# Optimization experiments

Measured on AMD Instinct MI355X. Metric: run time of the kernel, lower is better.

## Reference

```python
import jax, jax.numpy as jnp
import numpy as np

B, S, D_IN = 4, 2048, 2048
H, HD, G = 16, 128, 4
D_OUT = H * HD  # 2048
EPS = 1e-6
NEG_INF = -1e9


def zc_rmsnorm(x, scale):
    # zero-centered RMSNorm, computed in fp32
    xf = x.astype(jnp.float32)
    rms = jax.lax.rsqrt(jnp.mean(xf * xf, axis=-1, keepdims=True) + EPS)
    return (xf * rms * (1.0 + scale)).astype(x.dtype)


def rope(x, cos, sin):
    # x: (b, h, s, d); cos/sin: (s, d) -> broadcast over (b, h)
    d = x.shape[-1]
    x1, x2 = x[..., : d // 2], x[..., d // 2 :]
    rotated = jnp.concatenate([-x2, x1], axis=-1)
    return x * cos[None, None] + rotated * sin[None, None]


def setup_inputs() -> dict:
    key = jax.random.key(0)
    ks = jax.random.split(key, 8)
    x = jax.random.normal(ks[0], (B, S, D_IN), dtype=jnp.float32)
    # causal mask: True = masked out (upper triangle above diagonal)
    mask = jnp.triu(jnp.ones((S, S), dtype=bool), k=1)
    attn_mask = jnp.ones((B, S), dtype=bool)  # True = valid token
    # RoPE tables
    pos = jnp.arange(S, dtype=jnp.float32)
    inv = 1.0 / (10000.0 ** (jnp.arange(0, HD, 2, dtype=jnp.float32) / HD))
    ang = pos[:, None] * inv[None, :]              # (S, HD/2)
    ang = jnp.concatenate([ang, ang], axis=-1)     # (S, HD)
    cos, sin = jnp.cos(ang), jnp.sin(ang)
    s_in = 1.0 / np.sqrt(D_IN)
    Wq = jax.random.normal(ks[1], (D_IN, D_OUT), dtype=jnp.float32) * s_in
    Wk = jax.random.normal(ks[2], (D_IN, G * HD), dtype=jnp.float32) * s_in
    Wv = jax.random.normal(ks[3], (D_IN, G * HD), dtype=jnp.float32) * s_in
    Wg = jax.random.normal(ks[4], (D_IN, D_OUT), dtype=jnp.float32) * s_in
    Wo = jax.random.normal(ks[5], (D_OUT, D_IN), dtype=jnp.float32) / np.sqrt(D_OUT)
    q_scale = jnp.zeros((HD,), dtype=jnp.float32)
    k_scale = jnp.zeros((HD,), dtype=jnp.float32)
    return {"x": x, "mask": mask, "attn_mask": attn_mask, "cos": cos, "sin": sin,
            "Wq": Wq, "Wk": Wk, "Wv": Wv, "Wg": Wg, "Wo": Wo,
            "q_scale": q_scale, "k_scale": k_scale}


def reference(x, mask, attn_mask, cos, sin, Wq, Wk, Wv, Wg, Wo, q_scale, k_scale):
    b, s, _ = x.shape
    q = (x @ Wq).reshape(b, s, H, HD).transpose(0, 2, 1, 3)   # (b,H,s,hd)
    k = (x @ Wk).reshape(b, s, G, HD).transpose(0, 2, 1, 3)   # (b,G,s,hd)
    v = (x @ Wv).reshape(b, s, G, HD).transpose(0, 2, 1, 3)   # (b,G,s,hd)
    gate = jax.nn.sigmoid(x @ Wg)                             # (b,s,d_out)

    q = zc_rmsnorm(q, q_scale)
    k = zc_rmsnorm(k, k_scale)
    q = rope(q, cos[:s], sin[:s])
    k = rope(k, cos[:s], sin[:s])

    # GQA: repeat kv heads
    rep = H // G
    k = jnp.repeat(k, rep, axis=1)   # (b,H,s,hd)
    v = jnp.repeat(v, rep, axis=1)

    # combined mask: True = masked out
    curr = mask[:s, :s][None, None] | (~attn_mask[:, None, None, :s])  # (b,1,s,s)
    scores = jnp.einsum("bhqd,bhkd->bhqk", q, k) / np.sqrt(HD)
    scores = jnp.where(curr, NEG_INF, scores)
    attn = jax.nn.softmax(scores, axis=-1)
    ctx = jnp.einsum("bhqk,bhkd->bhqd", attn, v)              # (b,H,s,hd)
    ctx = ctx.transpose(0, 2, 1, 3).reshape(b, s, D_OUT)
    ctx = ctx * gate
    return ctx @ Wo
```

## Files before the change

### kernel.cpp

```cpp
#include <hip/hip_runtime.h>

typedef _Float16 half_t;
typedef _Float16 f16x8 __attribute__((ext_vector_type(8)));
typedef float    f32x4 __attribute__((ext_vector_type(4)));

typedef __attribute__((address_space(1))) const void void_g;
typedef __attribute__((address_space(3))) void void_l;
#define GLOAD_LDS16(gp, lp) __builtin_amdgcn_global_load_lds((void_g*)(gp), (void_l*)(lp), 16, 0, 0)

constexpr int B_ = 4, S_ = 2048, DIN_ = 2048, H_ = 16, HD_ = 128, G_ = 4, DOUT_ = 2048;
constexpr int NC_ = 5120;

__global__ __launch_bounds__(256) void cvt_f16(const float* __restrict__ in,
                                               half_t* __restrict__ out, int n4) {
  int i = blockIdx.x * blockDim.x + threadIdx.x;
  if (i < n4) {
    float4 v = reinterpret_cast<const float4*>(in)[i];
    union { half_t h[4]; uint2 u; } pk;
    pk.h[0] = (half_t)v.x; pk.h[1] = (half_t)v.y;
    pk.h[2] = (half_t)v.z; pk.h[3] = (half_t)v.w;
    reinterpret_cast<uint2*>(out)[i] = pk.u;
  }
}

__global__ __launch_bounds__(256) void transpose_cvt(const float* __restrict__ in,
                                                     half_t* __restrict__ out, int R, int C) {
  __shared__ float t[32][33];
  int tx = threadIdx.x, ty = threadIdx.y;
  int c0 = blockIdx.x * 32, r0 = blockIdx.y * 32;
#pragma unroll
  for (int i = ty; i < 32; i += 8) t[i][tx] = in[(size_t)(r0 + i) * C + c0 + tx];
  __syncthreads();
#pragma unroll
  for (int i = ty; i < 32; i += 8)
    out[(size_t)(c0 + i) * R + r0 + tx] = (half_t)t[tx][i];
}

__device__ __forceinline__ void storeC(half_t* p, float v) { *p = (half_t)v; }
__device__ __forceinline__ void storeC(float* p, float v)  { *p = v; }

#define BARRIER   asm volatile("s_barrier" ::: "memory")
#define LGKM0     asm volatile("s_waitcnt lgkmcnt(0)" ::: "memory"); __builtin_amdgcn_sched_barrier(0)
#define VMCNT3    asm volatile("s_waitcnt vmcnt(3)" ::: "memory")

template <typename OutT>
__global__ __launch_bounds__(512, 4) void gemm_bk32(const half_t* __restrict__ A,
                                                    const half_t* __restrict__ Bt,
                                                    OutT* __restrict__ C,
                                                    int M, int N, int K) {
  __shared__ alignas(16) half_t Ash[3][256 * 32];
  __shared__ alignas(16) half_t Bsh[3][128 * 32];
  const int tid  = threadIdx.x;
  const int lane = tid & 63;
  const int wid  = tid >> 6;
  const int lq = lane & 15, lg = lane >> 4;
  const int wm = wid >> 1, wn = wid & 1;

  const int gx = gridDim.x;
  int wgid = blockIdx.y * gx + blockIdx.x;
  const int chunk = (gx * gridDim.y) >> 3;
  wgid = (wgid & 7) * chunk + (wgid >> 3);
  const int mb = wgid / gx, nb = wgid - mb * gx;

  const int nk = K >> 5;

  const int arow0 = wid * 32 + (lane >> 2);
  const int arow1 = arow0 + 16;
  const int brow  = wid * 16 + (lane >> 2);
  const half_t* aSrc0 = A  + (size_t)(mb * 256 + arow0) * K + (((lane & 3) ^ ((arow0 >> 1) & 3)) << 3);
  const half_t* aSrc1 = A  + (size_t)(mb * 256 + arow1) * K + (((lane & 3) ^ ((arow1 >> 1) & 3)) << 3);
  const half_t* bSrc  = Bt + (size_t)(nb * 128 + brow)  * K + (((lane & 3) ^ ((brow  >> 1) & 3)) << 3);

  auto stage = [&](int kt, int bsel) {
    GLOAD_LDS16(aSrc0 + kt * 32, &Ash[bsel][wid * 1024]);
    GLOAD_LDS16(aSrc1 + kt * 32, &Ash[bsel][wid * 1024 + 512]);
    GLOAD_LDS16(bSrc  + kt * 32, &Bsh[bsel][wid * 512]);
  };

  f32x4 acc[4][4];
#pragma unroll
  for (int i = 0; i < 4; ++i)
#pragma unroll
    for (int j = 0; j < 4; ++j) acc[i][j] = (f32x4){0.f, 0.f, 0.f, 0.f};

  const int rdslot = (lg ^ ((lq >> 1) & 3)) * 8;

  stage(0, 0);
  stage(1, 1);
  VMCNT3;
  BARRIER;

  int cur = 0;
#pragma unroll 1
  for (int t = 0; t < nk; ++t) {
    {
      const int kt2 = (t + 2 < nk) ? t + 2 : nk - 1;
      int b2 = cur + 2; if (b2 >= 3) b2 -= 3;
      stage(kt2, b2);
    }
    f16x8 a4[4], b4[4];
#pragma unroll
    for (int mi = 0; mi < 4; ++mi)
      a4[mi] = *reinterpret_cast<const f16x8*>(&Ash[cur][(wm * 64 + mi * 16 + lq) * 32 + rdslot]);
#pragma unroll
    for (int nj = 0; nj < 4; ++nj)
      b4[nj] = *reinterpret_cast<const f16x8*>(&Bsh[cur][(wn * 64 + nj * 16 + lq) * 32 + rdslot]);
    LGKM0;
    __builtin_amdgcn_s_setprio(1);
#pragma unroll
    for (int mi = 0; mi < 4; ++mi)
#pragma unroll
      for (int nj = 0; nj < 4; ++nj)
        acc[mi][nj] = __builtin_amdgcn_mfma_f32_16x16x32_f16(a4[mi], b4[nj], acc[mi][nj], 0, 0, 0);
    __builtin_amdgcn_s_setprio(0);
    VMCNT3;
    BARRIER;
    cur = (cur == 2) ? 0 : cur + 1;
  }

#pragma unroll
  for (int mi = 0; mi < 4; ++mi) {
#pragma unroll
    for (int r = 0; r < 4; ++r) {
      const size_t row = (size_t)(mb * 256 + wm * 64 + mi * 16 + lg * 4 + r);
#pragma unroll
      for (int nj = 0; nj < 4; ++nj) {
        const int col = nb * 128 + wn * 64 + nj * 16 + lq;
        storeC(&C[row * N + col], acc[mi][nj][r]);
      }
    }
  }
}

__global__ __launch_bounds__(256) void post_qk(const half_t* __restrict__ QKVG,
                                               half_t* __restrict__ Q, half_t* __restrict__ Kd,
                                               const float* __restrict__ cosT,
                                               const float* __restrict__ sinT,
                                               const float* __restrict__ q_scale,
                                               const float* __restrict__ k_scale) {
  const int row  = blockIdx.x;
  const int slot = blockIdx.y * 4 + (threadIdx.x >> 6);
  const int lane = threadIdx.x & 63;
  const int b = row >> 11, s = row & (S_ - 1);
  const bool isq = slot < 16;
  const int col0 = isq ? slot * 128 : 2048 + (slot - 16) * 128;
  float x0 = (float)QKVG[(size_t)row * NC_ + col0 + lane];
  float x1 = (float)QKVG[(size_t)row * NC_ + col0 + lane + 64];
  float ss = x0 * x0 + x1 * x1;
#pragma unroll
  for (int m = 1; m < 64; m <<= 1) ss += __shfl_xor(ss, m);
  float rms = rsqrtf(ss * (1.f / 128.f) + 1e-6f);
  const float* sc = isq ? q_scale : k_scale;
  float y0 = x0 * rms * (1.f + sc[lane]);
  float y1 = x1 * rms * (1.f + sc[lane + 64]);
  float c0 = cosT[s * 128 + lane], c1 = cosT[s * 128 + lane + 64];
  float s0 = sinT[s * 128 + lane], s1 = sinT[s * 128 + lane + 64];
  float r0 = y0 * c0 - y1 * s0;
  float r1 = y1 * c1 + y0 * s1;
  if (isq) { r0 *= 0.12751743f; r1 *= 0.12751743f; }
  half_t* dst = isq ? (Q  + ((size_t)(b * H_ + slot) * S_ + s) * HD_)
                    : (Kd + ((size_t)(b * G_ + slot - 16) * S_ + s) * HD_);
  dst[lane]      = (half_t)r0;
  dst[lane + 64] = (half_t)r1;
}

__global__ __launch_bounds__(256) void v_transpose(const half_t* __restrict__ QKVG,
                                                   half_t* __restrict__ VT) {
  __shared__ half_t t[32][33];
  int tx = threadIdx.x, ty = threadIdx.y;
  int s0 = blockIdx.x * 32, d0 = blockIdx.y * 32;
  int bg = blockIdx.z;
  int b = bg >> 2, g = bg & 3;
#pragma unroll
  for (int i = ty; i < 32; i += 8)
    t[i][tx] = QKVG[(size_t)(b * S_ + s0 + i) * NC_ + 2560 + g * 128 + d0 + tx];
  __syncthreads();
#pragma unroll
  for (int i = ty; i < 32; i += 8)
    VT[((size_t)bg * 128 + d0 + i) * S_ + s0 + tx] = t[tx][i];
}

__global__ __launch_bounds__(256) void flash_attn4(const half_t* __restrict__ Q,
                                                   const half_t* __restrict__ K,
                                                   const half_t* __restrict__ VT,
                                                   const half_t* __restrict__ QKVG,
                                                   half_t* __restrict__ ctxg) {
  __shared__ alignas(16) half_t Klds[3][32 * 128];
  __shared__ alignas(16) half_t Vlds[3][128 * 32];
  __shared__ alignas(16) half_t Plds[4][2][16 * 40];

  const int lane = threadIdx.x & 63;
  const int wid  = threadIdx.x >> 6;
  const int lq = lane & 15, lg = lane >> 4;
  const int qa = blockIdx.x;
  const int h = blockIdx.y, b = blockIdx.z;
  const int g = h >> 2;

  const half_t* Kb = K  + ((size_t)(b * G_ + g) * S_) * HD_;
  const half_t* Vb = VT + ((size_t)(b * G_ + g) * HD_) * S_;

  auto stage = [&](int kb, int bsel) {
#pragma unroll
    for (int ii = 0; ii < 2; ++ii) {
      const int i = wid * 2 + ii;
      {
        const int row  = i * 4 + lg;
        const int csrc = (lq * 16) ^ ((row & 7) << 4);
        GLOAD_LDS16(Kb + (size_t)(kb + row) * HD_ + (csrc >> 1), &Klds[bsel][i * 512]);
      }
      {
        const int d    = i * 16 + (lane >> 2);
        const int csrc = ((lane & 3) * 16) ^ (((d >> 1) & 3) << 4);
        GLOAD_LDS16(Vb + (size_t)d * S_ + kb + (csrc >> 1), &Vlds[bsel][i * 512]);
      }
    }
  };

#pragma unroll 1
  for (int seg = 0; seg < 2; ++seg) {
    const int qt = seg ? (15 - qa) : qa;
    const int q0w = qt * 128 + wid * 32;
    const half_t* Qb = Q + ((size_t)(b * H_ + h) * S_ + q0w) * HD_;

    f16x8 qf[2][4];
#pragma unroll
    for (int qs = 0; qs < 2; ++qs)
#pragma unroll
      for (int kc = 0; kc < 4; ++kc)
        qf[qs][kc] = *reinterpret_cast<const f16x8*>(Qb + (size_t)(qs * 16 + lq) * HD_ + kc * 32 + lg * 8);

    f32x4 O[2][8];
#pragma unroll
    for (int qs = 0; qs < 2; ++qs)
#pragma unroll
      for (int nc = 0; nc < 8; ++nc) O[qs][nc] = (f32x4){0.f, 0.f, 0.f, 0.f};
    float lf[2] = {0.f, 0.f};

    const int nt = 4 * qt + 4;
    const int qmax = q0w + 31;

    if (seg) {
      asm volatile("s_waitcnt vmcnt(0)" ::: "memory");
      __builtin_amdgcn_s_barrier();
    }
    stage(0, 0);
    stage(32, 1);
    asm volatile("s_waitcnt vmcnt(4)" ::: "memory");
    __builtin_amdgcn_s_barrier();

    int cur = 0;
#pragma unroll 1
    for (int t = 0; t < nt; ++t) {
      {
        const int t2 = (t + 2 < nt) ? t + 2 : nt - 1;
        int b2 = cur + 2; if (b2 >= 3) b2 -= 3;
        stage(t2 * 32, b2);
      }
      const int kb = t * 32;
      if (kb <= qmax) {
        const half_t* kbuf = Klds[cur];
        const half_t* vbuf = Vlds[cur];
        f32x4 sA[2][2];
#pragma unroll
        for (int qs = 0; qs < 2; ++qs)
#pragma unroll
          for (int ks = 0; ks < 2; ++ks) sA[qs][ks] = (f32x4){0.f, 0.f, 0.f, 0.f};
        __builtin_amdgcn_s_setprio(1);
#pragma unroll
        for (int kc = 0; kc < 4; ++kc)
#pragma unroll
          for (int ks = 0; ks < 2; ++ks) {
            const int row = ks * 16 + lq;
            const int off = row * 128 + ((((kc * 64 + lg * 16)) ^ ((row & 7) << 4)) >> 1);
            f16x8 kf = *reinterpret_cast<const f16x8*>(kbuf + off);
            sA[0][ks] = __builtin_amdgcn_mfma_f32_16x16x32_f16(kf, qf[0][kc], sA[0][ks], 0, 0, 0);
            sA[1][ks] = __builtin_amdgcn_mfma_f32_16x16x32_f16(kf, qf[1][kc], sA[1][ks], 0, 0, 0);
          }
        __builtin_amdgcn_s_setprio(0);
        f16x8 pf[2];
#pragma unroll
        for (int qs = 0; qs < 2; ++qs) {
          const int qg = q0w + qs * 16 + lq;
          const bool diag = (kb + 31 > q0w + qs * 16);
          float rs = 0.f;
          union { half_t hh[8]; uint2 u2[2]; } pk;
#pragma unroll
          for (int ks = 0; ks < 2; ++ks)
#pragma unroll
            for (int r = 0; r < 4; ++r) {
              float sv = sA[qs][ks][r];
              if (diag) {
                const int key = kb + ks * 16 + lg * 4 + r;
                if (key > qg) sv = -1e9f;
              }
              const float p = __builtin_amdgcn_exp2f(sv - 1.5f);
              rs += p;
              pk.hh[ks * 4 + r] = (half_t)p;
            }
          lf[qs] += rs;
          half_t* Pw = &Plds[wid][qs][0];
          *reinterpret_cast<uint2*>(Pw + lq * 40 + lg * 4)      = pk.u2[0];
          *reinterpret_cast<uint2*>(Pw + lq * 40 + 16 + lg * 4) = pk.u2[1];
        }
        pf[0] = *reinterpret_cast<const f16x8*>(&Plds[wid][0][0] + lq * 40 + lg * 8);
        pf[1] = *reinterpret_cast<const f16x8*>(&Plds[wid][1][0] + lq * 40 + lg * 8);
        __builtin_amdgcn_s_setprio(1);
#pragma unroll
        for (int nc = 0; nc < 8; ++nc) {
          const int d = nc * 16 + lq;
          const int off = d * 32 + (((lg * 16) ^ (((d >> 1) & 3) << 4)) >> 1);
          f16x8 vf = *reinterpret_cast<const f16x8*>(vbuf + off);
          O[0][nc] = __builtin_amdgcn_mfma_f32_16x16x32_f16(vf, pf[0], O[0][nc], 0, 0, 0);
          O[1][nc] = __builtin_amdgcn_mfma_f32_16x16x32_f16(vf, pf[1], O[1][nc], 0, 0, 0);
        }
        __builtin_amdgcn_s_setprio(0);
      }
      asm volatile("s_waitcnt vmcnt(4)" ::: "memory");
      __builtin_amdgcn_s_barrier();
      cur = (cur == 2) ? 0 : cur + 1;
    }

#pragma unroll
    for (int qs = 0; qs < 2; ++qs) {
      float l = lf[qs];
      l += __shfl_xor(l, 16);
      l += __shfl_xor(l, 32);
      const float linv = 1.f / l;
      const int qg = q0w + qs * 16 + lq;
      const size_t row = (size_t)b * S_ + qg;
#pragma unroll
      for (int nc = 0; nc < 8; ++nc) {
        const int col = h * 128 + nc * 16 + lg * 4;
        union { uint2 u; half_t hh[4]; } gg;
        gg.u = *reinterpret_cast<const uint2*>(QKVG + row * NC_ + 3072 + col);
        union { half_t hh[4]; uint2 u; } ov;
#pragma unroll
        for (int r = 0; r < 4; ++r) {
          const float gate = 1.f / (1.f + __expf(-(float)gg.hh[r]));
          ov.hh[r] = (half_t)(O[qs][nc][r] * linv * gate);
        }
        *reinterpret_cast<uint2*>(ctxg + row * DOUT_ + col) = ov.u;
      }
    }
  }
}

extern "C" void kernel_launch(void* const* d_in, const int* in_sizes, int n_in,
                              void* d_out, int out_size, void* d_ws, size_t ws_size,
                              hipStream_t stream) {
  const float* x     = (const float*)d_in[0];
  const float* cosT  = (const float*)d_in[3];
  const float* sinT  = (const float*)d_in[4];
  const float* Wq    = (const float*)d_in[5];
  const float* Wk    = (const float*)d_in[6];
  const float* Wv    = (const float*)d_in[7];
  const float* Wg    = (const float*)d_in[8];
  const float* Wo    = (const float*)d_in[9];
  const float* q_scale = (const float*)d_in[10];
  const float* k_scale = (const float*)d_in[11];
  float* out = (float*)d_out;

  const size_t MB = 1ull << 20;
  char* w = (char*)d_ws;
  half_t* xh   = (half_t*)(w);
  half_t* ctxg = (half_t*)(w);
  half_t* WT   = (half_t*)(w + 32 * MB);
  half_t* WoT  = (half_t*)(w + 52 * MB);
  half_t* QKVG = (half_t*)(w + 60 * MB);
  half_t* Qh   = (half_t*)(w + 140 * MB);
  half_t* Kh   = (half_t*)(w + 172 * MB);
  half_t* VTh  = (half_t*)(w + 180 * MB);

  dim3 tb(32, 8);
  cvt_f16<<<16384, 256, 0, stream>>>(x, xh, B_ * S_ * DIN_ / 4);
  transpose_cvt<<<dim3(64, 64), tb, 0, stream>>>(Wq, WT,                     2048, 2048);
  transpose_cvt<<<dim3(16, 64), tb, 0, stream>>>(Wk, WT + 2048 * 2048,       2048, 512);
  transpose_cvt<<<dim3(16, 64), tb, 0, stream>>>(Wv, WT + 2560 * 2048,       2048, 512);
  transpose_cvt<<<dim3(64, 64), tb, 0, stream>>>(Wg, WT + (size_t)3072 * 2048, 2048, 2048);
  transpose_cvt<<<dim3(64, 64), tb, 0, stream>>>(Wo, WoT,                    2048, 2048);

  gemm_bk32<half_t><<<dim3(40, 32), 512, 0, stream>>>(xh, WT, QKVG, 8192, NC_, 2048);

  post_qk<<<dim3(8192, 5), 256, 0, stream>>>(QKVG, Qh, Kh, cosT, sinT, q_scale, k_scale);
  v_transpose<<<dim3(64, 4, 16), tb, 0, stream>>>(QKVG, VTh);

  flash_attn4<<<dim3(8, 16, 4), 256, 0, stream>>>(Qh, Kh, VTh, QKVG, ctxg);

  gemm_bk32<float><<<dim3(16, 32), 512, 0, stream>>>(ctxg, WoT, out, 8192, 2048, 2048);
}
```

Measured before the change: 494.9 us.

## Load GEMM B operand directly into registers instead of staging through LDS

The shared GEMM kernel now keeps only the A tile in the triple-buffered LDS ring. Each wave loads its B fragments straight from global memory into registers, one k-step ahead. This removes the B LDS buffers and the LDS reads for B, and shrinks LDS use. In exchange, the four waves that share a column block load the same B data separately, and global-load latency is hidden by only a one-iteration register prefetch with a new combined waitcnt scheme.

```diff
diff --git a/kernel.cpp b/kernel.cpp
--- a/kernel.cpp
+++ b/kernel.cpp
@@ -40,16 +40,13 @@
 __device__ __forceinline__ void storeC(float* p, float v)  { *p = v; }
 
 #define BARRIER   asm volatile("s_barrier" ::: "memory")
-#define LGKM0     asm volatile("s_waitcnt lgkmcnt(0)" ::: "memory"); __builtin_amdgcn_sched_barrier(0)
-#define VMCNT3    asm volatile("s_waitcnt vmcnt(3)" ::: "memory")
 
 template <typename OutT>
-__global__ __launch_bounds__(512, 4) void gemm_bk32(const half_t* __restrict__ A,
+__global__ __launch_bounds__(512, 4) void gemm_breg(const half_t* __restrict__ A,
                                                     const half_t* __restrict__ Bt,
                                                     OutT* __restrict__ C,
                                                     int M, int N, int K) {
   __shared__ alignas(16) half_t Ash[3][256 * 32];
-  __shared__ alignas(16) half_t Bsh[3][128 * 32];
   const int tid  = threadIdx.x;
   const int lane = tid & 63;
   const int wid  = tid >> 6;
@@ -66,17 +63,27 @@
 
   const int arow0 = wid * 32 + (lane >> 2);
   const int arow1 = arow0 + 16;
-  const int brow  = wid * 16 + (lane >> 2);
-  const half_t* aSrc0 = A  + (size_t)(mb * 256 + arow0) * K + (((lane & 3) ^ ((arow0 >> 1) & 3)) << 3);
-  const half_t* aSrc1 = A  + (size_t)(mb * 256 + arow1) * K + (((lane & 3) ^ ((arow1 >> 1) & 3)) << 3);
-  const half_t* bSrc  = Bt + (size_t)(nb * 128 + brow)  * K + (((lane & 3) ^ ((brow  >> 1) & 3)) << 3);
-
-  auto stage = [&](int kt, int bsel) {
+  const half_t* aSrc0 = A + (size_t)(mb * 256 + arow0) * K + (((lane & 3) ^ ((arow0 >> 1) & 3)) << 3);
+  const half_t* aSrc1 = A + (size_t)(mb * 256 + arow1) * K + (((lane & 3) ^ ((arow1 >> 1) & 3)) << 3);
+
+  auto stageA = [&](int kt, int bsel) {
     GLOAD_LDS16(aSrc0 + kt * 32, &Ash[bsel][wid * 1024]);
     GLOAD_LDS16(aSrc1 + kt * 32, &Ash[bsel][wid * 1024 + 512]);
-    GLOAD_LDS16(bSrc  + kt * 32, &Bsh[bsel][wid * 512]);
   };
 
+  const half_t* bP0 = Bt + (size_t)(nb * 128 + wn * 64 + lq) * K + lg * 8;
+  const half_t* bP1 = bP0 + (size_t)16 * K;
+  const half_t* bP2 = bP0 + (size_t)32 * K;
+  const half_t* bP3 = bP0 + (size_t)48 * K;
+
+  f16x8 b4[4];
+  auto loadB = [&](int kt) {
+    b4[0] = *reinterpret_cast<const f16x8*>(bP0 + kt * 32);
+    b4[1] = *reinterpret_cast<const f16x8*>(bP1 + kt * 32);
+    b4[2] = *reinterpret_cast<const f16x8*>(bP2 + kt * 32);
+    b4[3] = *reinterpret_cast<const f16x8*>(bP3 + kt * 32);
+  };
+
   f32x4 acc[4][4];
 #pragma unroll
   for (int i = 0; i < 4; ++i)
@@ -85,27 +92,26 @@
 
   const int rdslot = (lg ^ ((lq >> 1) & 3)) * 8;
 
-  stage(0, 0);
-  stage(1, 1);
-  VMCNT3;
+  stageA(0, 0);
+  stageA(1, 1);
+  asm volatile("s_waitcnt vmcnt(0)" ::: "memory");
   BARRIER;
+  loadB(0);
 
   int cur = 0;
 #pragma unroll 1
   for (int t = 0; t < nk; ++t) {
+    f16x8 a4[4];
+#pragma unroll
+    for (int mi = 0; mi < 4; ++mi)
+      a4[mi] = *reinterpret_cast<const f16x8*>(&Ash[cur][(wm * 64 + mi * 16 + lq) * 32 + rdslot]);
     {
       const int kt2 = (t + 2 < nk) ? t + 2 : nk - 1;
       int b2 = cur + 2; if (b2 >= 3) b2 -= 3;
-      stage(kt2, b2);
-    }
-    f16x8 a4[4], b4[4];
-#pragma unroll
-    for (int mi = 0; mi < 4; ++mi)
-      a4[mi] = *reinterpret_cast<const f16x8*>(&Ash[cur][(wm * 64 + mi * 16 + lq) * 32 + rdslot]);
-#pragma unroll
-    for (int nj = 0; nj < 4; ++nj)
-      b4[nj] = *reinterpret_cast<const f16x8*>(&Bsh[cur][(wn * 64 + nj * 16 + lq) * 32 + rdslot]);
-    LGKM0;
+      stageA(kt2, b2);
+    }
+    asm volatile("s_waitcnt lgkmcnt(0) vmcnt(2)" ::: "memory");
+    __builtin_amdgcn_sched_barrier(0);
     __builtin_amdgcn_s_setprio(1);
 #pragma unroll
     for (int mi = 0; mi < 4; ++mi)
@@ -113,7 +119,10 @@
       for (int nj = 0; nj < 4; ++nj)
         acc[mi][nj] = __builtin_amdgcn_mfma_f32_16x16x32_f16(a4[mi], b4[nj], acc[mi][nj], 0, 0, 0);
     __builtin_amdgcn_s_setprio(0);
-    VMCNT3;
+    {
+      const int kt1 = (t + 1 < nk) ? t + 1 : nk - 1;
+      loadB(kt1);
+    }
     BARRIER;
     cur = (cur == 2) ? 0 : cur + 1;
   }
@@ -379,12 +388,12 @@
   transpose_cvt<<<dim3(64, 64), tb, 0, stream>>>(Wg, WT + (size_t)3072 * 2048, 2048, 2048);
   transpose_cvt<<<dim3(64, 64), tb, 0, stream>>>(Wo, WoT,                    2048, 2048);
 
-  gemm_bk32<half_t><<<dim3(40, 32), 512, 0, stream>>>(xh, WT, QKVG, 8192, NC_, 2048);
+  gemm_breg<half_t><<<dim3(40, 32), 512, 0, stream>>>(xh, WT, QKVG, 8192, NC_, 2048);
 
   post_qk<<<dim3(8192, 5), 256, 0, stream>>>(QKVG, Qh, Kh, cosT, sinT, q_scale, k_scale);
   v_transpose<<<dim3(64, 4, 16), tb, 0, stream>>>(QKVG, VTh);
 
   flash_attn4<<<dim3(8, 16, 4), 256, 0, stream>>>(Qh, Kh, VTh, QKVG, ctxg);
 
-  gemm_bk32<float><<<dim3(16, 32), 512, 0, stream>>>(ctxg, WoT, out, 8192, 2048, 2048);
-}
+  gemm_breg<float><<<dim3(16, 32), 512, 0, stream>>>(ctxg, WoT, out, 8192, 2048, 2048);
+}
```

New measurement: 715.5 us. 1.45x slower.
